# Optimization experiments

Hardware: AMD Instinct MI355X
Metric: run time of the kernel (lower is better)

## Reference

```python
import jax, jax.numpy as jnp
import numpy as np

G, N, H = 32, 128, 32
EDGE_ATTR_DIM = 16
NUM_SPATIAL = 512
NUM_EDGE_DIS = 128
MAX_DIST = 5
N_EDGES = 65536
N_PATHS = 1048576
N_LAYERS = 12


def setup_inputs() -> dict:
    key = jax.random.key(0)
    ks = jax.random.split(key, 8)
    rng = np.random.default_rng(0)
    attn_bias = jax.random.normal(ks[0], (G, N + 1, N + 1), jnp.float32)
    spatial_pos = jax.random.randint(ks[1], (G, N, N), 0, NUM_SPATIAL, jnp.int32)
    # unique (g,i,j) edge destinations -> deterministic scatter
    flat_e = rng.permutation(G * N * N)[:N_EDGES]
    g = flat_e // (N * N)
    rest = flat_e % (N * N)
    edge_index = jnp.asarray(np.stack([g, rest // N, rest % N]), jnp.int32)
    edge_attr = jax.random.normal(ks[2], (N_EDGES, EDGE_ATTR_DIM), jnp.float32)
    # unique (g,i,j,d) path destinations
    flat_p = rng.permutation(G * N * N * MAX_DIST)[:N_PATHS]
    pg = flat_p // (N * N * MAX_DIST)
    r = flat_p % (N * N * MAX_DIST)
    pi = r // (N * MAX_DIST)
    r = r % (N * MAX_DIST)
    pj = r // MAX_DIST
    pd = r % MAX_DIST
    src = rng.integers(0, N, N_PATHS)
    dst = rng.integers(0, N, N_PATHS)
    path_index = jnp.asarray(np.stack([pg, pi, pj, pd, src, dst]), jnp.int32)
    std = 0.02 / np.sqrt(N_LAYERS)
    edge_enc_w = jax.random.normal(ks[3], (H, EDGE_ATTR_DIM), jnp.float32) * std
    spatial_pos_emb = (jax.random.normal(ks[4], (NUM_SPATIAL, H), jnp.float32) * 0.02).at[0].set(0.0)  # padding_idx=0
    virt_dist = jax.random.normal(ks[5], (1, H), jnp.float32) * 0.02
    edge_dis_emb = jax.random.normal(ks[6], (NUM_EDGE_DIS * H * H, 1), jnp.float32) * 0.02
    return dict(attn_bias=attn_bias, spatial_pos=spatial_pos, edge_index=edge_index,
                edge_attr=edge_attr, path_index=path_index, edge_enc_w=edge_enc_w,
                spatial_pos_emb=spatial_pos_emb, virt_dist=virt_dist,
                edge_dis_emb=edge_dis_emb, max_dist=MAX_DIST)


def reference(attn_bias, spatial_pos, edge_index, edge_attr, path_index,
              edge_enc_w, spatial_pos_emb, virt_dist, edge_dis_emb, max_dist):
    n_graph, n1, _ = attn_bias.shape
    n_node = n1 - 1
    num_heads = edge_enc_w.shape[0]
    # [G, H, N+1, N+1] base bias (repeat over heads)
    gab = jnp.broadcast_to(attn_bias[:, None], (n_graph, num_heads, n1, n1))
    # spatial position bias: embedding lookup [G,N,N,H] -> [G,H,N,N]
    spb = jnp.transpose(spatial_pos_emb[spatial_pos], (0, 3, 1, 2))
    gab = gab.at[:, :, 1:, 1:].add(spb)
    t = virt_dist.reshape(1, num_heads, 1)
    gab = gab.at[:, :, 1:, 0].add(t)
    gab = gab.at[:, :, 0, :].add(t)
    # edge encoder: [E, edge_attr_dim] @ [edge_attr_dim, H] -> [E, H]
    ea = edge_attr @ edge_enc_w.T
    dense_adj = jnp.zeros((n_graph, n_node, n_node, num_heads), ea.dtype)
    dense_adj = dense_adj.at[edge_index[0], edge_index[1], edge_index[2]].set(ea)
    # multi-hop path features: scatter gathered edges into [G,N,N,D,H]
    edge_input = jnp.zeros((n_graph, n_node, n_node, max_dist, num_heads), ea.dtype)
    gathered = dense_adj[path_index[0], path_index[4], path_index[5]]
    edge_input = edge_input.at[path_index[0], path_index[1], path_index[2], path_index[3]].set(gathered)
    # path length normalizer
    sp = jnp.where(spatial_pos == 0, 1, spatial_pos)
    sp = jnp.where(sp > 1, sp - 1, sp)
    sp = jnp.clip(sp, 0, max_dist)
    # per-distance head mixing: [D, G*N*N, H] x [D, H, H]
    flat = jnp.transpose(edge_input, (3, 0, 1, 2, 4)).reshape(max_dist, -1, num_heads)
    W = edge_dis_emb.reshape(-1, num_heads, num_heads)[:max_dist]
    flat = jnp.einsum('dnh,dhk->dnk', flat, W)
    ei = flat.reshape(max_dist, n_graph, n_node, n_node, num_heads).transpose(1, 2, 3, 0, 4)
    ei = (ei.sum(-2) / sp[..., None].astype(ei.dtype)).transpose(0, 3, 1, 2)
    gab = gab.at[:, :, 1:, 1:].add(ei)
    return gab + attn_bias[:, None]
```

## Files before the change

### kernel.cpp

```cpp
#include <hip/hip_runtime.h>

#define G_    32
#define N_    128
#define NP1_  129
#define H_    32
#define EAD_  16
#define MAXD_ 5
#define NE_   65536
#define NPTH_ 1048576

__global__ __launch_bounds__(256) void edge_encode_kernel(
    const float* __restrict__ edge_attr,
    const int*   __restrict__ edge_index,
    const float* __restrict__ edge_enc_w,
    float*       __restrict__ eaval,
    int*         __restrict__ edge_map) {
  int t = blockIdx.x * blockDim.x + threadIdx.x;
  if (t >= NE_ * H_) return;
  int e = t >> 5;
  int h = t & 31;
  const float* ea = edge_attr + e * EAD_;
  const float* w  = edge_enc_w + h * EAD_;
  float s = 0.f;
#pragma unroll
  for (int k = 0; k < EAD_; ++k) s += ea[k] * w[k];
  eaval[t] = s;
  if (h == 0) {
    int g = edge_index[e];
    int i = edge_index[NE_ + e];
    int j = edge_index[2 * NE_ + e];
    edge_map[(g * N_ + i) * N_ + j] = e + 1;
  }
}

__global__ __launch_bounds__(256) void path_scatter_kernel(
    const int* __restrict__ path_index,
    const int* __restrict__ edge_map,
    int*       __restrict__ slot) {
  int p = blockIdx.x * blockDim.x + threadIdx.x;
  int pg = path_index[p];
  int pi = path_index[NPTH_ + p];
  int pj = path_index[2 * NPTH_ + p];
  int pd = path_index[3 * NPTH_ + p];
  int ps = path_index[4 * NPTH_ + p];
  int pt = path_index[5 * NPTH_ + p];
  int m = edge_map[(pg * N_ + ps) * N_ + pt];
  if (m) {
    slot[((pg * N_ + pi) * N_ + pj) * MAXD_ + pd] = m;
  }
}

__global__ __launch_bounds__(256) void output_fused_kernel(
    const float* __restrict__ attn_bias,
    const int*   __restrict__ spatial_pos,
    const float* __restrict__ spe,
    const float* __restrict__ virt,
    const int*   __restrict__ slot,
    const float* __restrict__ eaval,
    const float* __restrict__ Wdis,
    float*       __restrict__ out) {
  __shared__ float lds_val[N_ * 33];
  __shared__ float lds_virt[H_];
  __shared__ int   q[N_ * MAXD_];
  __shared__ int   q_cnt;

  int blk = blockIdx.x;
  int g = blk / NP1_;
  int a = blk - g * NP1_;
  int tid = threadIdx.x;

  if (tid < H_) lds_virt[tid] = virt[tid];

  const float* ab = attn_bias + (g * NP1_ + a) * NP1_;

  if (a == 0) {
    __syncthreads();
    for (int t = tid; t < H_ * NP1_; t += 256) {
      int h = t / NP1_;
      int b = t - h * NP1_;
      out[((g * H_ + h) * NP1_) * NP1_ + b] = 2.f * ab[b] + lds_virt[h];
    }
    return;
  }

  int i = a - 1;
  const int* sp_row   = spatial_pos + (g * N_ + i) * N_;
  const int* slot_row = slot + (size_t)((g * N_ + i) * N_) * MAXD_;

  for (int t = tid; t < N_ * 33; t += 256) lds_val[t] = 0.f;
  if (tid == 0) q_cnt = 0;
  __syncthreads();

  for (int f = tid; f < N_ * MAXD_; f += 256) {
    int m = slot_row[f];
    if (m) {
      int j = f / MAXD_;
      int d = f - j * MAXD_;
      int idx = atomicAdd(&q_cnt, 1);
      q[idx] = (j << 19) | (d << 16) | (m - 1);
    }
  }
  __syncthreads();
  int cnt = q_cnt;

  int grp  = tid >> 5;
  int lane = tid & 31;
  for (int s = grp; s < cnt; s += 8) {
    int ent = q[s];
    int j = ent >> 19;
    int d = (ent >> 16) & 7;
    int e = ent & 0xFFFF;
    const float* ea = eaval + (size_t)e * H_;
    const float* Wd = Wdis + d * (H_ * H_);
    float v0 = 0.f, v1 = 0.f, v2 = 0.f, v3 = 0.f;
#pragma unroll
    for (int h = 0; h < H_; h += 4) {
      v0 += ea[h + 0] * Wd[(h + 0) * H_ + lane];
      v1 += ea[h + 1] * Wd[(h + 1) * H_ + lane];
      v2 += ea[h + 2] * Wd[(h + 2) * H_ + lane];
      v3 += ea[h + 3] * Wd[(h + 3) * H_ + lane];
    }
    atomicAdd(&lds_val[j * 33 + lane], (v0 + v1) + (v2 + v3));
  }
  __syncthreads();

  for (int t = tid; t < N_ * H_; t += 256) {
    int j = t >> 5;
    int h = t & 31;
    int s = sp_row[j];
    int s2 = (s == 0) ? 1 : s;
    s2 = (s2 > 1) ? s2 - 1 : s2;
    s2 = (s2 > MAXD_) ? MAXD_ : s2;
    float inv = (s2 == 1) ? 1.0f
              : (s2 == 2) ? 0.5f
              : (s2 == 3) ? (1.0f / 3.0f)
              : (s2 == 4) ? 0.25f : 0.2f;
    lds_val[j * 33 + h] = spe[s * H_ + h] + lds_val[j * 33 + h] * inv;
  }
  __syncthreads();

  for (int t = tid; t < H_ * NP1_; t += 256) {
    int h = t / NP1_;
    int b = t - h * NP1_;
    float val = 2.f * ab[b];
    if (b == 0) {
      val += lds_virt[h];
    } else {
      val += lds_val[(b - 1) * 33 + h];
    }
    out[((g * H_ + h) * NP1_ + a) * NP1_ + b] = val;
  }
}

extern "C" void kernel_launch(void* const* d_in, const int* in_sizes, int n_in,
                              void* d_out, int out_size, void* d_ws, size_t ws_size,
                              hipStream_t stream) {
  const float* attn_bias   = (const float*)d_in[0];
  const int*   spatial_pos = (const int*)d_in[1];
  const int*   edge_index  = (const int*)d_in[2];
  const float* edge_attr   = (const float*)d_in[3];
  const int*   path_index  = (const int*)d_in[4];
  const float* edge_enc_w  = (const float*)d_in[5];
  const float* spe         = (const float*)d_in[6];
  const float* virt        = (const float*)d_in[7];
  const float* edge_dis    = (const float*)d_in[8];
  float* out = (float*)d_out;

  const size_t SLOT_ELEMS = (size_t)G_ * N_ * N_ * MAXD_;
  const size_t MAP_ELEMS  = (size_t)G_ * N_ * N_;

  int*   slot     = (int*)d_ws;
  int*   edge_map = slot + SLOT_ELEMS;
  float* eaval    = (float*)(edge_map + MAP_ELEMS);

  hipMemsetAsync(slot, 0, (SLOT_ELEMS + MAP_ELEMS) * sizeof(int), stream);

  {
    int total = NE_ * H_;
    edge_encode_kernel<<<(total + 255) / 256, 256, 0, stream>>>(
        edge_attr, edge_index, edge_enc_w, eaval, edge_map);
  }
  path_scatter_kernel<<<NPTH_ / 256, 256, 0, stream>>>(
      path_index, edge_map, slot);
  output_fused_kernel<<<G_ * NP1_, 256, 0, stream>>>(
      attn_bias, spatial_pos, spe, virt, slot, eaval, edge_dis, out);
}
```

Before: 92.09 us.

## Split output into bf16 intermediate mix kernel and grid-stride streaming writer

Replaces the fused per-row output kernel with two kernels. The first computes the mixed edge and spatial values per half-row and stores them in a bf16 intermediate laid out [G,N,H,N]. The second is a grid-stride kernel that writes the full output contiguously by adding twice the attention bias to either the virtual distance or the unpacked bf16 value. The aim is fully coalesced output stores and more parallel blocks. The cost is an extra kernel launch, an intermediate round trip through memory, and bf16 rounding of the bias values, which may break tolerance.

```diff
diff --git a/kernel.cpp b/kernel.cpp
--- a/kernel.cpp
+++ b/kernel.cpp
@@ -8,6 +8,13 @@
 #define MAXD_ 5
 #define NE_   65536
 #define NPTH_ 1048576
+#define HALF_ 64
+
+static __device__ __forceinline__ unsigned int f2bf(float f) {
+  unsigned int u = __float_as_uint(f);
+  u += 0x7fffu + ((u >> 16) & 1u);
+  return u >> 16;
+}
 
 __global__ __launch_bounds__(256) void edge_encode_kernel(
     const float* __restrict__ edge_attr,
@@ -50,54 +57,35 @@
   }
 }
 
-__global__ __launch_bounds__(256) void output_fused_kernel(
-    const float* __restrict__ attn_bias,
+__global__ __launch_bounds__(256) void mix_half_kernel(
+    const int*   __restrict__ slot,
     const int*   __restrict__ spatial_pos,
     const float* __restrict__ spe,
-    const float* __restrict__ virt,
-    const int*   __restrict__ slot,
     const float* __restrict__ eaval,
     const float* __restrict__ Wdis,
-    float*       __restrict__ out) {
-  __shared__ float lds_val[N_ * 33];
-  __shared__ float lds_virt[H_];
-  __shared__ int   q[N_ * MAXD_];
+    unsigned short* __restrict__ valmid) {
+  __shared__ float lds_val[HALF_ * 33];
+  __shared__ int   q[HALF_ * MAXD_];
   __shared__ int   q_cnt;
 
   int blk = blockIdx.x;
-  int g = blk / NP1_;
-  int a = blk - g * NP1_;
+  int c   = blk & 1;
+  int gi  = blk >> 1;
+  int j0  = c * HALF_;
   int tid = threadIdx.x;
 
-  if (tid < H_) lds_virt[tid] = virt[tid];
-
-  const float* ab = attn_bias + (g * NP1_ + a) * NP1_;
-
-  if (a == 0) {
-    __syncthreads();
-    for (int t = tid; t < H_ * NP1_; t += 256) {
-      int h = t / NP1_;
-      int b = t - h * NP1_;
-      out[((g * H_ + h) * NP1_) * NP1_ + b] = 2.f * ab[b] + lds_virt[h];
-    }
-    return;
-  }
-
-  int i = a - 1;
-  const int* sp_row   = spatial_pos + (g * N_ + i) * N_;
-  const int* slot_row = slot + (size_t)((g * N_ + i) * N_) * MAXD_;
-
-  for (int t = tid; t < N_ * 33; t += 256) lds_val[t] = 0.f;
+  for (int t = tid; t < HALF_ * 33; t += 256) lds_val[t] = 0.f;
   if (tid == 0) q_cnt = 0;
   __syncthreads();
 
-  for (int f = tid; f < N_ * MAXD_; f += 256) {
-    int m = slot_row[f];
+  const int* srow = slot + ((size_t)gi * N_ + j0) * MAXD_;
+  for (int f = tid; f < HALF_ * MAXD_; f += 256) {
+    int m = srow[f];
     if (m) {
-      int j = f / MAXD_;
-      int d = f - j * MAXD_;
+      int jl = f / MAXD_;
+      int d  = f - jl * MAXD_;
       int idx = atomicAdd(&q_cnt, 1);
-      q[idx] = (j << 19) | (d << 16) | (m - 1);
+      q[idx] = (jl << 19) | (d << 16) | (m - 1);
     }
   }
   __syncthreads();
@@ -107,9 +95,9 @@
   int lane = tid & 31;
   for (int s = grp; s < cnt; s += 8) {
     int ent = q[s];
-    int j = ent >> 19;
-    int d = (ent >> 16) & 7;
-    int e = ent & 0xFFFF;
+    int jl = ent >> 19;
+    int d  = (ent >> 16) & 7;
+    int e  = ent & 0xFFFF;
     const float* ea = eaval + (size_t)e * H_;
     const float* Wd = Wdis + d * (H_ * H_);
     float v0 = 0.f, v1 = 0.f, v2 = 0.f, v3 = 0.f;
@@ -120,14 +108,15 @@
       v2 += ea[h + 2] * Wd[(h + 2) * H_ + lane];
       v3 += ea[h + 3] * Wd[(h + 3) * H_ + lane];
     }
-    atomicAdd(&lds_val[j * 33 + lane], (v0 + v1) + (v2 + v3));
-  }
-  __syncthreads();
-
-  for (int t = tid; t < N_ * H_; t += 256) {
-    int j = t >> 5;
-    int h = t & 31;
-    int s = sp_row[j];
+    atomicAdd(&lds_val[jl * 33 + lane], (v0 + v1) + (v2 + v3));
+  }
+  __syncthreads();
+
+  const int* sp_row = spatial_pos + (size_t)gi * N_ + j0;
+  for (int t = tid; t < HALF_ * H_; t += 256) {
+    int jl = t >> 5;
+    int h  = t & 31;
+    int s = sp_row[jl];
     int s2 = (s == 0) ? 1 : s;
     s2 = (s2 > 1) ? s2 - 1 : s2;
     s2 = (s2 > MAXD_) ? MAXD_ : s2;
@@ -135,20 +124,47 @@
               : (s2 == 2) ? 0.5f
               : (s2 == 3) ? (1.0f / 3.0f)
               : (s2 == 4) ? 0.25f : 0.2f;
-    lds_val[j * 33 + h] = spe[s * H_ + h] + lds_val[j * 33 + h] * inv;
-  }
-  __syncthreads();
-
-  for (int t = tid; t < H_ * NP1_; t += 256) {
-    int h = t / NP1_;
-    int b = t - h * NP1_;
-    float val = 2.f * ab[b];
-    if (b == 0) {
-      val += lds_virt[h];
+    lds_val[jl * 33 + h] = spe[s * H_ + h] + lds_val[jl * 33 + h] * inv;
+  }
+  __syncthreads();
+
+  unsigned short* vbase = valmid + ((size_t)gi * H_) * N_ + j0;
+  for (int u = tid; u < H_ * (HALF_ / 2); u += 256) {
+    int h  = u >> 5;
+    int jp = u & 31;
+    int jl = jp * 2;
+    unsigned int lo = f2bf(lds_val[jl * 33 + h]);
+    unsigned int hi = f2bf(lds_val[(jl + 1) * 33 + h]);
+    *(unsigned int*)(vbase + (size_t)h * N_ + jl) = lo | (hi << 16);
+  }
+}
+
+__global__ __launch_bounds__(256) void stream_out_kernel(
+    const float* __restrict__ attn_bias,
+    const float* __restrict__ virt,
+    const unsigned short* __restrict__ valmid,
+    float* __restrict__ out) {
+  const int PLANE = NP1_ * NP1_;
+  const int TOT = G_ * H_ * PLANE;
+  int stride = gridDim.x * blockDim.x;
+  for (int idx = blockIdx.x * blockDim.x + threadIdx.x; idx < TOT;
+       idx += stride) {
+    int gh = idx / PLANE;
+    int r  = idx - gh * PLANE;
+    int a  = r / NP1_;
+    int b  = r - a * NP1_;
+    int g  = gh >> 5;
+    int h  = gh & 31;
+    float base = 2.f * attn_bias[g * PLANE + r];
+    float add;
+    if (a == 0 || b == 0) {
+      add = virt[h];
     } else {
-      val += lds_val[(b - 1) * 33 + h];
+      unsigned short v =
+          valmid[((size_t)(g * N_ + (a - 1)) * H_ + h) * N_ + (b - 1)];
+      add = __uint_as_float((unsigned int)v << 16);
     }
-    out[((g * H_ + h) * NP1_ + a) * NP1_ + b] = val;
+    out[idx] = base + add;
   }
 }
 
@@ -168,20 +184,21 @@
 
   const size_t SLOT_ELEMS = (size_t)G_ * N_ * N_ * MAXD_;
   const size_t MAP_ELEMS  = (size_t)G_ * N_ * N_;
-
-  int*   slot     = (int*)d_ws;
-  int*   edge_map = slot + SLOT_ELEMS;
-  float* eaval    = (float*)(edge_map + MAP_ELEMS);
+  const size_t EAV_ELEMS  = (size_t)NE_ * H_;
+
+  int*            slot     = (int*)d_ws;
+  int*            edge_map = slot + SLOT_ELEMS;
+  float*          eaval    = (float*)(edge_map + MAP_ELEMS);
+  unsigned short* valmid   = (unsigned short*)(eaval + EAV_ELEMS);
 
   hipMemsetAsync(slot, 0, (SLOT_ELEMS + MAP_ELEMS) * sizeof(int), stream);
 
-  {
-    int total = NE_ * H_;
-    edge_encode_kernel<<<(total + 255) / 256, 256, 0, stream>>>(
-        edge_attr, edge_index, edge_enc_w, eaval, edge_map);
-  }
+  edge_encode_kernel<<<(NE_ * H_ + 255) / 256, 256, 0, stream>>>(
+      edge_attr, edge_index, edge_enc_w, eaval, edge_map);
   path_scatter_kernel<<<NPTH_ / 256, 256, 0, stream>>>(
       path_index, edge_map, slot);
-  output_fused_kernel<<<G_ * NP1_, 256, 0, stream>>>(
-      attn_bias, spatial_pos, spe, virt, slot, eaval, edge_dis, out);
-}
+  mix_half_kernel<<<G_ * N_ * 2, 256, 0, stream>>>(
+      slot, spatial_pos, spe, eaval, edge_dis, valmid);
+  stream_out_kernel<<<2048, 256, 0, stream>>>(
+      attn_bias, virt, valmid, out);
+}
```

Result: slower. 120.1 us (+30.4%).
